# Kernel tuning notes

Hardware: AMD Instinct MI355X
Metric: run time of the kernel (lower is better)

Reference implementation:

```python
import jax, jax.numpy as jnp
import numpy as np

EMBED_DIM = 512
NUM_HEADS = 16
WIN = (8, 8)
N_TOK = WIN[0] * WIN[1]           # 64 tokens per window
HEAD_DIM = EMBED_DIM // NUM_HEADS  # 32
SCALE = HEAD_DIM ** -0.5
B_WIN = 1024                       # batch * num_windows
NUM_WINDOWS = 256                  # windows per image -> batch images = 4


def _relative_bias_index(window_size):
    wh, ww = window_size
    coords = np.stack(np.meshgrid(np.arange(wh), np.arange(ww), indexing='ij'))  # (2, wh, ww)
    flat = coords.reshape(2, -1)                                   # (2, N)
    rel = (flat[:, :, None] - flat[:, None, :]).transpose(1, 2, 0)  # (N, N, 2)
    rel[:, :, 0] += wh - 1
    rel[:, :, 1] += ww - 1
    rel[:, :, 0] *= 2 * ww - 1
    return rel.sum(-1)  # (N, N) int


def setup_inputs() -> dict:
    key = jax.random.key(0)
    ks = jax.random.split(key, 6)
    x = jax.random.normal(ks[0], (B_WIN, N_TOK, EMBED_DIM), dtype=jnp.float32)
    attention_mask = jax.random.normal(ks[1], (NUM_WINDOWS, N_TOK, N_TOK), dtype=jnp.float32)
    qkv_w = jax.random.normal(ks[2], (EMBED_DIM, 3 * EMBED_DIM), dtype=jnp.float32) * 0.02
    qkv_b = jnp.zeros((3 * EMBED_DIM,), dtype=jnp.float32)
    proj_w = jax.random.normal(ks[3], (EMBED_DIM, EMBED_DIM), dtype=jnp.float32) * 0.02
    proj_b = jnp.zeros((EMBED_DIM,), dtype=jnp.float32)
    n_bias = (2 * WIN[0] - 1) * (2 * WIN[1] - 1)  # 225
    bias_table = jax.random.normal(ks[4], (n_bias, NUM_HEADS), dtype=jnp.float32) * 0.02
    rel_index = jnp.asarray(_relative_bias_index(WIN), dtype=jnp.int32)  # (N, N)
    return {"x": x, "attention_mask": attention_mask, "qkv_w": qkv_w, "qkv_b": qkv_b,
            "proj_w": proj_w, "proj_b": proj_b, "bias_table": bias_table, "rel_index": rel_index}


def reference(x, attention_mask, qkv_w, qkv_b, proj_w, proj_b, bias_table, rel_index):
    B, N, C = x.shape
    nw = attention_mask.shape[0]
    bimg = B // nw
    qkv = x @ qkv_w + qkv_b                              # (B, N, 3C)
    # original rearrange 'b n (h d c) -> d b n h c' groups last dim as (heads, 3, head_dim)
    qkv = qkv.reshape(B, N, NUM_HEADS, 3, HEAD_DIM)
    q, k, v = qkv[..., 0, :], qkv[..., 1, :], qkv[..., 2, :]  # each (B, N, H, hd)
    attn = jnp.einsum('bqhd,bkhd->bhqk', q, k) * SCALE        # (B, H, N, N)
    bias = bias_table[rel_index].transpose(2, 0, 1)           # (H, N, N)
    attn = attn + bias[None]
    attn = attn.reshape(bimg, nw, NUM_HEADS, N, N) + attention_mask[None, :, None]
    attn = jax.nn.softmax(attn, axis=-1).reshape(B, NUM_HEADS, N, N)
    out = jnp.einsum('bhqk,bkhd->bqhd', attn, v).reshape(B, N, C)
    return out @ proj_w + proj_b
```

## Files before the change

kernel.cpp:

```cpp
#include <hip/hip_runtime.h>
#include <hip/hip_bf16.h>


typedef unsigned short u16;
typedef __bf16 bx8 __attribute__((ext_vector_type(8)));
typedef float f4_t __attribute__((ext_vector_type(4)));

#define QKV_ELEMS 33554432ull
#define SCALE 0.17677669529663687f

static __device__ __forceinline__ u16 f2b(float f) {
    return __builtin_bit_cast(u16, (__bf16)f);
}

typedef const unsigned int __attribute__((address_space(1)))* gas_t;
typedef unsigned int __attribute__((address_space(3)))* las_t;
static __device__ __forceinline__ void glds16(const void* g, void* l) {
    __builtin_amdgcn_global_load_lds((gas_t)g, (las_t)l, 16, 0, 0);
}

__global__ void cvt_k(const float* __restrict__ X, u16* __restrict__ Xb) {
    size_t i = ((size_t)blockIdx.x * 256 + threadIdx.x) * 8;
    float4 v0 = *(const float4*)(X + i);
    float4 v1 = *(const float4*)(X + i + 4);
    ushort4 p0, p1;
    p0.x = f2b(v0.x); p0.y = f2b(v0.y); p0.z = f2b(v0.z); p0.w = f2b(v0.w);
    p1.x = f2b(v1.x); p1.y = f2b(v1.y); p1.z = f2b(v1.z); p1.w = f2b(v1.w);
    *(ushort4*)(Xb + i) = p0;
    *(ushort4*)(Xb + i + 4) = p1;
}

__global__ void wt_k(const float* __restrict__ W, u16* __restrict__ Wt,
                     int K, int N) {
    int idx = blockIdx.x * 256 + threadIdx.x;
    if (idx >= N * K) return;
    int n = idx / K, k = idx - n * K;
    Wt[idx] = f2b(W[(size_t)k * N + n]);
}

__global__ void bias_k(const float* __restrict__ bias_table,
                       const int* __restrict__ rel_index,
                       float* __restrict__ bias_full) {
    int idx = blockIdx.x * 256 + threadIdx.x;
    int h = idx >> 12, rc = idx & 4095;
    bias_full[idx] = bias_table[rel_index[rc] * 16 + h];
}

template <int MODE>
__global__ __launch_bounds__(256) void gemm_k(
    const u16* __restrict__ A, const u16* __restrict__ Bt,
    const float* __restrict__ bias, void* __restrict__ Out, int K) {
    const int tid  = threadIdx.x;
    const int wave = tid >> 6, lane = tid & 63;
    const int quad = lane >> 4, l16 = lane & 15;
    const int wm = wave >> 1, wn = wave & 1;
    const int m0 = blockIdx.y * 128, n0 = blockIdx.x * 128;

    __shared__ alignas(16) char smem[17408];
    u16* a_s = (u16*)smem;
    u16* b_s = (u16*)(smem + 8192);

    const int lr = lane >> 2, lc = (lane & 3) * 8;
    const int w16 = wave * 16;

    f4_t acc[4][4];
#pragma unroll
    for (int i = 0; i < 4; ++i)
#pragma unroll
        for (int j = 0; j < 4; ++j) acc[i][j] = (f4_t){0.f, 0.f, 0.f, 0.f};

    for (int kt = 0; kt < K; kt += 32) {
        if (MODE == 0) {
            const u16* Ab = A + (size_t)m0 * K + kt;
            glds16(Ab + (size_t)(w16 + lr) * K + lc,      &a_s[w16 * 32]);
            glds16(Ab + (size_t)(w16 + 64 + lr) * K + lc, &a_s[(w16 + 64) * 32]);
        } else {
            const u16* Ab = A + (((size_t)(kt >> 5) * 1024 + (m0 >> 6)) << 11);
            glds16(Ab + ((w16 + lr) << 5) + lc,        &a_s[w16 * 32]);
            glds16(Ab + 2048 + ((w16 + lr) << 5) + lc, &a_s[(w16 + 64) * 32]);
        }
        const u16* Bb = Bt + (size_t)n0 * K + kt;
        glds16(Bb + (size_t)(w16 + lr) * K + lc,      &b_s[w16 * 32]);
        glds16(Bb + (size_t)(w16 + 64 + lr) * K + lc, &b_s[(w16 + 64) * 32]);
        __syncthreads();

        bx8 af[4], bfr[4];
#pragma unroll
        for (int mt = 0; mt < 4; ++mt)
            af[mt] = *(const bx8*)&a_s[(wm * 64 + mt * 16 + l16) * 32 + quad * 8];
#pragma unroll
        for (int nt = 0; nt < 4; ++nt)
            bfr[nt] = *(const bx8*)&b_s[(wn * 64 + nt * 16 + l16) * 32 + quad * 8];
#pragma unroll
        for (int mt = 0; mt < 4; ++mt)
#pragma unroll
            for (int nt = 0; nt < 4; ++nt)
                acc[mt][nt] = __builtin_amdgcn_mfma_f32_16x16x32_bf16(
                    af[mt], bfr[nt], acc[mt][nt], 0, 0, 0);
        __syncthreads();
    }

    float bv[4];
#pragma unroll
    for (int nt = 0; nt < 4; ++nt) bv[nt] = bias[n0 + wn * 64 + nt * 16 + l16];

    if (MODE == 0) {
        u16* c_s = (u16*)smem;
        u16* qkv = (u16*)Out;
        const int g = tid >> 6, s = tid & 63;
        const int cgb = n0 + g * 32;
        const int h = cgb / 96, rr = cgb - h * 96;
        const int which = rr >> 5;
#pragma unroll
        for (int p = 0; p < 2; ++p) {
            if (wm == p) {
#pragma unroll
                for (int mt = 0; mt < 4; ++mt)
#pragma unroll
                    for (int nt = 0; nt < 4; ++nt)
#pragma unroll
                        for (int i = 0; i < 4; ++i)
                            c_s[(mt * 16 + quad * 4 + i) * 136 +
                                wn * 64 + nt * 16 + l16] =
                                f2b(acc[mt][nt][i] + bv[nt]);
            }
            __syncthreads();
            const int w = (m0 >> 6) + p;
            u16* dst = qkv + (size_t)which * QKV_ELEMS +
                       ((size_t)((w << 4) + h) << 11);
#pragma unroll
            for (int j = 0; j < 4; ++j) {
                int idx = s + 64 * j;
                int tok = idx >> 2, d8 = (idx & 3) * 8;
                uint4 v = *(const uint4*)&c_s[tok * 136 + g * 32 + d8];
                *(uint4*)(dst + idx * 8) = v;
            }
            __syncthreads();
        }
    } else {
        float* c_sf = (float*)smem;
        float* Of = (float*)Out;
#pragma unroll
        for (int p = 0; p < 4; ++p) {
            if (wm == (p >> 1)) {
                const int mtb = (p & 1) * 2;
#pragma unroll
                for (int mt2 = 0; mt2 < 2; ++mt2)
#pragma unroll
                    for (int nt = 0; nt < 4; ++nt)
#pragma unroll
                        for (int i = 0; i < 4; ++i)
                            c_sf[(mt2 * 16 + quad * 4 + i) * 136 +
                                 wn * 64 + nt * 16 + l16] =
                                acc[mtb + mt2][nt][i] + bv[nt];
            }
            __syncthreads();
#pragma unroll
            for (int j = 0; j < 4; ++j) {
                int fl = tid + 256 * j;
                int row = fl >> 5, c4 = (fl & 31) * 4;
                float4 v = *(const float4*)&c_sf[row * 136 + c4];
                *(float4*)&Of[(size_t)(m0 + p * 32 + row) * 512 + n0 + c4] = v;
            }
            __syncthreads();
        }
    }
}

__global__ __launch_bounds__(256) void attn_k(
    const u16* __restrict__ qkv, const float* __restrict__ mask,
    const float* __restrict__ biasf, u16* __restrict__ attn_out) {
    const int bx = blockIdx.x;
    const int w = bx >> 4, h = bx & 15;
    const int wmk = w & 255;
    const int tid = threadIdx.x;
    const int wave = tid >> 6, lane = tid & 63;
    const int quad = lane >> 4, l16 = lane & 15;

    __shared__ alignas(16) u16 q_s[64 * 40];
    __shared__ alignas(16) u16 k_s[64 * 40];
    __shared__ alignas(16) u16 vT[32 * 72];
    __shared__ alignas(16) float s_s[64 * 68];
    __shared__ alignas(16) u16 p_s[64 * 72];

    const size_t base = (size_t)((w << 4) + h) * 2048;
    {
        int tok = tid >> 2, d0 = (tid & 3) * 8;
        uint4 qv = *(const uint4*)(qkv + base + tid * 8);
        *(uint4*)&q_s[tok * 40 + d0] = qv;
        uint4 kv = *(const uint4*)(qkv + QKV_ELEMS + base + tid * 8);
        *(uint4*)&k_s[tok * 40 + d0] = kv;
        uint4 vv = *(const uint4*)(qkv + 2 * QKV_ELEMS + base + tid * 8);
        const u16* pv = (const u16*)&vv;
#pragma unroll
        for (int j = 0; j < 8; ++j) vT[(d0 + j) * 72 + tok] = pv[j];
    }
    __syncthreads();

    {
        bx8 a = *(const bx8*)&q_s[(wave * 16 + l16) * 40 + quad * 8];
#pragma unroll
        for (int nt = 0; nt < 4; ++nt) {
            bx8 b = *(const bx8*)&k_s[(nt * 16 + l16) * 40 + quad * 8];
            f4_t acc = (f4_t){0.f, 0.f, 0.f, 0.f};
            acc = __builtin_amdgcn_mfma_f32_16x16x32_bf16(a, b, acc, 0, 0, 0);
#pragma unroll
            for (int i = 0; i < 4; ++i) {
                int r = wave * 16 + quad * 4 + i;
                int c = nt * 16 + l16;
                float s = acc[i] * SCALE + biasf[(h << 12) + (r << 6) + c] +
                          mask[((size_t)wmk * 64 + r) * 64 + c];
                s_s[r * 68 + c] = s;
            }
        }
    }
    __syncthreads();

    {
        int row = tid >> 2, j = (tid & 3) * 16;
        float mx = -1e30f;
#pragma unroll
        for (int cc = 0; cc < 16; ++cc) mx = fmaxf(mx, s_s[row * 68 + j + cc]);
        mx = fmaxf(mx, __shfl_xor(mx, 1));
        mx = fmaxf(mx, __shfl_xor(mx, 2));
        float e[16], sum = 0.f;
#pragma unroll
        for (int cc = 0; cc < 16; ++cc) {
            e[cc] = __expf(s_s[row * 68 + j + cc] - mx);
            sum += e[cc];
        }
        sum += __shfl_xor(sum, 1);
        sum += __shfl_xor(sum, 2);
        float inv = 1.f / sum;
#pragma unroll
        for (int cc = 0; cc < 16; ++cc) p_s[row * 72 + j + cc] = f2b(e[cc] * inv);
    }
    __syncthreads();

    {
        u16* os = (u16*)s_s;
#pragma unroll
        for (int nt = 0; nt < 2; ++nt) {
            f4_t acc = (f4_t){0.f, 0.f, 0.f, 0.f};
#pragma unroll
            for (int ks = 0; ks < 2; ++ks) {
                bx8 a = *(const bx8*)&p_s[(wave * 16 + l16) * 72 + ks * 32 + quad * 8];
                bx8 b = *(const bx8*)&vT[(nt * 16 + l16) * 72 + ks * 32 + quad * 8];
                acc = __builtin_amdgcn_mfma_f32_16x16x32_bf16(a, b, acc, 0, 0, 0);
            }
#pragma unroll
            for (int i = 0; i < 4; ++i)
                os[(wave * 16 + quad * 4 + i) * 40 + nt * 16 + l16] =
                    f2b(acc[i]);
        }
        __syncthreads();
        int tok = tid >> 2, d8 = (tid & 3) * 8;
        uint4 v = *(const uint4*)&os[tok * 40 + d8];
        *(uint4*)(attn_out + ((((size_t)h << 10) + w) << 11) + tid * 8) = v;
    }
}

extern "C" void kernel_launch(void* const* d_in, const int* in_sizes, int n_in,
                              void* d_out, int out_size, void* d_ws,
                              size_t ws_size, hipStream_t stream) {
    const float* x      = (const float*)d_in[0];
    const float* mask   = (const float*)d_in[1];
    const float* qkv_w  = (const float*)d_in[2];
    const float* qkv_b  = (const float*)d_in[3];
    const float* proj_w = (const float*)d_in[4];
    const float* proj_b = (const float*)d_in[5];
    const float* bias_t = (const float*)d_in[6];
    const int*   rel    = (const int*)d_in[7];
    float* out = (float*)d_out;

    char* ws = (char*)d_ws;
    u16* Wt1 = (u16*)ws;      ws += (size_t)1536 * 512 * 2;
    u16* Wt2 = (u16*)ws;      ws += (size_t)512 * 512 * 2;
    float* biasf = (float*)ws; ws += (size_t)16 * 64 * 64 * 4;
    u16* qkv = (u16*)ws;      ws += 3 * QKV_ELEMS * 2;
    u16* attn = (u16*)ws;     ws += QKV_ELEMS * 2;
    u16* xb = attn;

    cvt_k<<<16384, 256, 0, stream>>>(x, xb);
    wt_k<<<3072, 256, 0, stream>>>(qkv_w, Wt1, 512, 1536);
    wt_k<<<1024, 256, 0, stream>>>(proj_w, Wt2, 512, 512);
    bias_k<<<256, 256, 0, stream>>>(bias_t, rel, biasf);
    gemm_k<0><<<dim3(12, 512), 256, 0, stream>>>(xb, Wt1, qkv_b, qkv, 512);
    attn_k<<<16384, 256, 0, stream>>>(qkv, mask, biasf, attn);
    gemm_k<1><<<dim3(4, 512), 256, 0, stream>>>(attn, Wt2, proj_b, out, 512);
}
```

Baseline: 549.4 us.

## Replace GEMM with 256x256-tile, 4-stage pipelined, LDS-swizzled MFMA kernel

Both projection GEMMs move from a 128x128 tile with one synchronous LDS stage to a 256x256 tile with 512 threads, a 4-deep ring of async global-to-LDS stages with explicit vmcnt waits, XOR-swizzled LDS layout, s_setprio around MFMA bursts, and a block-id swizzle for L2 locality. The aim is to hide global load latency behind MFMA work and cut per-iteration barriers and bank conflicts. The kernel now uses 128KB of dynamic LDS, which limits occupancy to one block per CU. The K loop is hardcoded to 16 steps (K=512).

```diff
diff --git a/kernel.cpp b/kernel.cpp
--- a/kernel.cpp
+++ b/kernel.cpp
@@ -46,59 +46,120 @@
     bias_full[idx] = bias_table[rel_index[rc] * 16 + h];
 }
 
+
+#define MF(av, mt)                                                            \
+    acc[mt][0] = __builtin_amdgcn_mfma_f32_16x16x32_bf16(av, b0, acc[mt][0],  \
+                                                         0, 0, 0);            \
+    acc[mt][1] = __builtin_amdgcn_mfma_f32_16x16x32_bf16(av, b1, acc[mt][1],  \
+                                                         0, 0, 0);            \
+    acc[mt][2] = __builtin_amdgcn_mfma_f32_16x16x32_bf16(av, b2, acc[mt][2],  \
+                                                         0, 0, 0);            \
+    acc[mt][3] = __builtin_amdgcn_mfma_f32_16x16x32_bf16(av, b3, acc[mt][3],  \
+                                                         0, 0, 0);
+
+#define TILE_STEP(T, DOSTAGE, VMC)                                            \
+    {                                                                         \
+        const char* aT = ldsA + ((T) & 3) * 16384 + wm * 8192 + foff;         \
+        const char* bT = ldsB + ((T) & 3) * 16384 + wn * 4096 + foff;         \
+        bx8 b0 = *(const bx8*)(bT);                                           \
+        bx8 b1 = *(const bx8*)(bT + 1024);                                    \
+        bx8 b2 = *(const bx8*)(bT + 2048);                                    \
+        bx8 b3 = *(const bx8*)(bT + 3072);                                    \
+        bx8 a0 = *(const bx8*)(aT);                                           \
+        bx8 a1 = *(const bx8*)(aT + 1024);                                    \
+        bx8 a2 = *(const bx8*)(aT + 2048);                                    \
+        bx8 a3 = *(const bx8*)(aT + 3072);                                    \
+        if (DOSTAGE) STAGE_A((T) + 3);                                        \
+        __builtin_amdgcn_s_barrier();                                         \
+        __builtin_amdgcn_s_setprio(1);                                        \
+        MF(a0, 0) MF(a1, 1) MF(a2, 2) MF(a3, 3)                               \
+        __builtin_amdgcn_s_setprio(0);                                        \
+        __builtin_amdgcn_s_barrier();                                         \
+        bx8 a4 = *(const bx8*)(aT + 4096);                                    \
+        bx8 a5 = *(const bx8*)(aT + 5120);                                    \
+        bx8 a6 = *(const bx8*)(aT + 6144);                                    \
+        bx8 a7 = *(const bx8*)(aT + 7168);                                    \
+        if (DOSTAGE) STAGE_B((T) + 3);                                        \
+        if ((VMC) == 8) asm volatile("s_waitcnt vmcnt(8)" ::: "memory");      \
+        else if ((VMC) == 4) asm volatile("s_waitcnt vmcnt(4)" ::: "memory"); \
+        else if ((VMC) == 0) asm volatile("s_waitcnt vmcnt(0)" ::: "memory"); \
+        __builtin_amdgcn_s_barrier();                                         \
+        __builtin_amdgcn_s_setprio(1);                                        \
+        MF(a4, 4) MF(a5, 5) MF(a6, 6) MF(a7, 7)                               \
+        __builtin_amdgcn_s_setprio(0);                                        \
+        __builtin_amdgcn_s_barrier();                                         \
+    }
+
 template <int MODE>
-__global__ __launch_bounds__(256) void gemm_k(
+__global__ __launch_bounds__(512, 2) void gemm256_k(
     const u16* __restrict__ A, const u16* __restrict__ Bt,
-    const float* __restrict__ bias, void* __restrict__ Out, int K) {
-    const int tid  = threadIdx.x;
+    const float* __restrict__ bias, void* __restrict__ Out) {
+    extern __shared__ __align__(16) char smem[];
+    const int tid = threadIdx.x;
     const int wave = tid >> 6, lane = tid & 63;
-    const int quad = lane >> 4, l16 = lane & 15;
-    const int wm = wave >> 1, wn = wave & 1;
-    const int m0 = blockIdx.y * 128, n0 = blockIdx.x * 128;
-
-    __shared__ alignas(16) char smem[17408];
-    u16* a_s = (u16*)smem;
-    u16* b_s = (u16*)(smem + 8192);
-
-    const int lr = lane >> 2, lc = (lane & 3) * 8;
-    const int w16 = wave * 16;
-
-    f4_t acc[4][4];
-#pragma unroll
-    for (int i = 0; i < 4; ++i)
+    const int l16 = lane & 15, quad = lane >> 4;
+    const int wm = wave >> 2, wn = wave & 3;
+
+    const int NT_COL = (MODE == 0) ? 6 : 2;
+    const int NWG = (MODE == 0) ? 1536 : 512;
+    const int bid = blockIdx.x;
+    const int swz = (bid & 7) * (NWG >> 3) + (bid >> 3);
+    const int m0 = (swz / NT_COL) << 8;
+    const int n0 = (swz % NT_COL) << 8;
+
+    char* const ldsA = smem;
+    char* const ldsB = smem + 65536;
+
+    const int lr = lane >> 2, lc = lane & 3;
+    const int swzc = (lc ^ (lr & 3)) * 8;
+    const int stoff = wave * 1024;
+
+    const u16* Asrc0;
+    const u16* Asrc1;
+    if (MODE == 0) {
+        const int r0 = m0 + wave * 16 + lr;
+        Asrc0 = A + (size_t)r0 * 512 + swzc;
+        Asrc1 = Asrc0 + (size_t)128 * 512;
+    } else {
+        const int r0 = m0 + wave * 16 + lr, r1 = r0 + 128;
+        Asrc0 = A + (size_t)(r0 >> 6) * 2048 + (r0 & 63) * 32 + swzc;
+        Asrc1 = A + (size_t)(r1 >> 6) * 2048 + (r1 & 63) * 32 + swzc;
+    }
+    const u16* Bsrc0 = Bt + (size_t)(n0 + wave * 16 + lr) * 512 + swzc;
+    const u16* Bsrc1 = Bsrc0 + (size_t)128 * 512;
+
+    auto STAGE_A = [&](int T) {
+        char* d = ldsA + (T & 3) * 16384 + stoff;
+        if (MODE == 0) {
+            glds16(Asrc0 + T * 32, d);
+            glds16(Asrc1 + T * 32, d + 8192);
+        } else {
+            glds16(Asrc0 + (size_t)T * 2097152, d);
+            glds16(Asrc1 + (size_t)T * 2097152, d + 8192);
+        }
+    };
+    auto STAGE_B = [&](int T) {
+        char* d = ldsB + (T & 3) * 16384 + stoff;
+        glds16(Bsrc0 + T * 32, d);
+        glds16(Bsrc1 + T * 32, d + 8192);
+    };
+
+    const int foff = l16 * 64 + ((quad ^ (l16 & 3)) * 16);
+
+    f4_t acc[8][4];
+#pragma unroll
+    for (int i = 0; i < 8; ++i)
 #pragma unroll
         for (int j = 0; j < 4; ++j) acc[i][j] = (f4_t){0.f, 0.f, 0.f, 0.f};
 
-    for (int kt = 0; kt < K; kt += 32) {
-        if (MODE == 0) {
-            const u16* Ab = A + (size_t)m0 * K + kt;
-            glds16(Ab + (size_t)(w16 + lr) * K + lc,      &a_s[w16 * 32]);
-            glds16(Ab + (size_t)(w16 + 64 + lr) * K + lc, &a_s[(w16 + 64) * 32]);
-        } else {
-            const u16* Ab = A + (((size_t)(kt >> 5) * 1024 + (m0 >> 6)) << 11);
-            glds16(Ab + ((w16 + lr) << 5) + lc,        &a_s[w16 * 32]);
-            glds16(Ab + 2048 + ((w16 + lr) << 5) + lc, &a_s[(w16 + 64) * 32]);
-        }
-        const u16* Bb = Bt + (size_t)n0 * K + kt;
-        glds16(Bb + (size_t)(w16 + lr) * K + lc,      &b_s[w16 * 32]);
-        glds16(Bb + (size_t)(w16 + 64 + lr) * K + lc, &b_s[(w16 + 64) * 32]);
-        __syncthreads();
-
-        bx8 af[4], bfr[4];
-#pragma unroll
-        for (int mt = 0; mt < 4; ++mt)
-            af[mt] = *(const bx8*)&a_s[(wm * 64 + mt * 16 + l16) * 32 + quad * 8];
-#pragma unroll
-        for (int nt = 0; nt < 4; ++nt)
-            bfr[nt] = *(const bx8*)&b_s[(wn * 64 + nt * 16 + l16) * 32 + quad * 8];
-#pragma unroll
-        for (int mt = 0; mt < 4; ++mt)
-#pragma unroll
-            for (int nt = 0; nt < 4; ++nt)
-                acc[mt][nt] = __builtin_amdgcn_mfma_f32_16x16x32_bf16(
-                    af[mt], bfr[nt], acc[mt][nt], 0, 0, 0);
-        __syncthreads();
-    }
+    STAGE_A(0); STAGE_B(0); STAGE_A(1); STAGE_B(1); STAGE_A(2); STAGE_B(2);
+    asm volatile("s_waitcnt vmcnt(8)" ::: "memory");
+    __builtin_amdgcn_s_barrier();
+
+    for (int T = 0; T < 13; ++T) TILE_STEP(T, true, 8);
+    TILE_STEP(13, false, 4);
+    TILE_STEP(14, false, 0);
+    TILE_STEP(15, false, -1);
 
     float bv[4];
 #pragma unroll
@@ -106,34 +167,34 @@
 
     if (MODE == 0) {
         u16* c_s = (u16*)smem;
-        u16* qkv = (u16*)Out;
-        const int g = tid >> 6, s = tid & 63;
-        const int cgb = n0 + g * 32;
-        const int h = cgb / 96, rr = cgb - h * 96;
-        const int which = rr >> 5;
+        u16* qkvp = (u16*)Out;
+        const int cg = n0 + wave * 32;
+        const int hh = cg / 96;
+        const int which = (cg - hh * 96) >> 5;
+        u16* plane = qkvp + (size_t)which * QKV_ELEMS + (size_t)hh * 2048;
 #pragma unroll
         for (int p = 0; p < 2; ++p) {
             if (wm == p) {
 #pragma unroll
-                for (int mt = 0; mt < 4; ++mt)
+                for (int mt = 0; mt < 8; ++mt)
 #pragma unroll
                     for (int nt = 0; nt < 4; ++nt)
 #pragma unroll
                         for (int i = 0; i < 4; ++i)
-                            c_s[(mt * 16 + quad * 4 + i) * 136 +
+                            c_s[(mt * 16 + quad * 4 + i) * 264 +
                                 wn * 64 + nt * 16 + l16] =
                                 f2b(acc[mt][nt][i] + bv[nt]);
             }
             __syncthreads();
-            const int w = (m0 >> 6) + p;
-            u16* dst = qkv + (size_t)which * QKV_ELEMS +
-                       ((size_t)((w << 4) + h) << 11);
-#pragma unroll
-            for (int j = 0; j < 4; ++j) {
-                int idx = s + 64 * j;
-                int tok = idx >> 2, d8 = (idx & 3) * 8;
-                uint4 v = *(const uint4*)&c_s[tok * 136 + g * 32 + d8];
-                *(uint4*)(dst + idx * 8) = v;
+#pragma unroll
+            for (int j = 0; j < 8; ++j) {
+                int row = j * 16 + (lane >> 2);
+                int gm = m0 + p * 128 + row;
+                int w_win = gm >> 6, tok = gm & 63;
+                uint4 v = *(const uint4*)&c_s[row * 264 + wave * 32 +
+                                              (lane & 3) * 8];
+                *(uint4*)(plane + (size_t)w_win * 32768 + tok * 32 +
+                          (lane & 3) * 8) = v;
             }
             __syncthreads();
         }
@@ -143,24 +204,24 @@
 #pragma unroll
         for (int p = 0; p < 4; ++p) {
             if (wm == (p >> 1)) {
-                const int mtb = (p & 1) * 2;
-#pragma unroll
-                for (int mt2 = 0; mt2 < 2; ++mt2)
+                const int mtb = (p & 1) * 4;
+#pragma unroll
+                for (int mt2 = 0; mt2 < 4; ++mt2)
 #pragma unroll
                     for (int nt = 0; nt < 4; ++nt)
 #pragma unroll
                         for (int i = 0; i < 4; ++i)
-                            c_sf[(mt2 * 16 + quad * 4 + i) * 136 +
+                            c_sf[(mt2 * 16 + quad * 4 + i) * 264 +
                                  wn * 64 + nt * 16 + l16] =
                                 acc[mtb + mt2][nt][i] + bv[nt];
             }
             __syncthreads();
 #pragma unroll
-            for (int j = 0; j < 4; ++j) {
-                int fl = tid + 256 * j;
-                int row = fl >> 5, c4 = (fl & 31) * 4;
-                float4 v = *(const float4*)&c_sf[row * 136 + c4];
-                *(float4*)&Of[(size_t)(m0 + p * 32 + row) * 512 + n0 + c4] = v;
+            for (int j = 0; j < 8; ++j) {
+                int flat = tid + 512 * j;
+                int r = flat >> 6, c4 = (flat & 63) * 4;
+                float4 v = *(const float4*)&c_sf[r * 264 + c4];
+                *(float4*)&Of[(size_t)(m0 + p * 64 + r) * 512 + n0 + c4] = v;
             }
             __syncthreads();
         }
@@ -285,7 +346,7 @@
     wt_k<<<3072, 256, 0, stream>>>(qkv_w, Wt1, 512, 1536);
     wt_k<<<1024, 256, 0, stream>>>(proj_w, Wt2, 512, 512);
     bias_k<<<256, 256, 0, stream>>>(bias_t, rel, biasf);
-    gemm_k<0><<<dim3(12, 512), 256, 0, stream>>>(xb, Wt1, qkv_b, qkv, 512);
+    gemm256_k<0><<<1536, 512, 131072, stream>>>(xb, Wt1, qkv_b, qkv);
     attn_k<<<16384, 256, 0, stream>>>(qkv, mask, biasf, attn);
-    gemm_k<1><<<dim3(4, 512), 256, 0, stream>>>(attn, Wt2, proj_b, out, 512);
-}
+    gemm256_k<1><<<512, 512, 131072, stream>>>(attn, Wt2, proj_b, out);
+}
```

Result: faster. 511.4 us (-6.9%).
